# Optimization experiments

Measured on AMD Instinct MI355X. Metric: run time of the kernel, lower is better.

## Reference

```python
import jax, jax.numpy as jnp
import numpy as np

IMG = 128      # raster_settings.image_size
FOCAL = 1.5    # simple pinhole projection (camera transform)
EPS = 1e-8
B, V, F = 4, 600, 1000


def setup_inputs() -> dict:
    key = jax.random.key(0)
    k1, k2 = jax.random.split(key)
    u = jax.random.uniform(k1, (B, V, 3), dtype=jnp.float32)
    xy = u[..., :2] * 2.0 - 1.0          # x,y in [-1, 1]
    z = u[..., 2:3] * 2.0 + 1.0          # z in [1, 3] (in front of camera)
    verts = jnp.concatenate([xy, z], axis=-1)   # [B, V, 3] world coords
    faces = jax.random.randint(k2, (F, 3), 0, V)  # [F, 3] vertex indices
    return {"verts": verts, "faces": faces}


def _pix_grid(H, W):
    # PyTorch3D NDC convention: +X left, +Y up; pixel centers at (2i+1)/S - 1 flipped.
    xs = 1.0 - (2.0 * jnp.arange(W, dtype=jnp.float32) + 1.0) / W
    ys = 1.0 - (2.0 * jnp.arange(H, dtype=jnp.float32) + 1.0) / H
    px = jnp.broadcast_to(xs[None, :], (H, W)).reshape(-1)  # [P]
    py = jnp.broadcast_to(ys[:, None], (H, W)).reshape(-1)  # [P]
    return px, py


def _edge(ax, ay, bx, by, px, py):
    # signed (twice-)area of triangle (a, b, p)
    return (bx - ax) * (py - ay) - (by - ay) * (px - ax)


def _seg_dist2(px, py, ax, ay, bx, by):
    # squared distance from point p to segment (a, b); all args broadcastable
    ex, ey = bx - ax, by - ay
    dx, dy = px - ax, py - ay
    ee = jnp.maximum(ex * ex + ey * ey, EPS)
    t = jnp.clip((dx * ex + dy * ey) / ee, 0.0, 1.0)
    rx = dx - t * ex
    ry = dy - t * ey
    return rx * rx + ry * ry


def _rasterize_one(v_ndc, faces, H, W):
    fv = v_ndc[faces]                       # [F, 3, 3] face vertices (ndc x, y, view z)
    v0, v1, v2 = fv[:, 0], fv[:, 1], fv[:, 2]
    px, py = _pix_grid(H, W)                # [P], P = H*W
    pxr, pyr = px[None, :], py[None, :]
    # signed face area [F]
    area = _edge(v0[:, 0], v0[:, 1], v1[:, 0], v1[:, 1], v2[:, 0], v2[:, 1])
    # edge functions at every pixel -> unnormalized barycentrics [F, P]
    w0 = _edge(v1[:, 0:1], v1[:, 1:2], v2[:, 0:1], v2[:, 1:2], pxr, pyr)
    w1 = _edge(v2[:, 0:1], v2[:, 1:2], v0[:, 0:1], v0[:, 1:2], pxr, pyr)
    w2 = _edge(v0[:, 0:1], v0[:, 1:2], v1[:, 0:1], v1[:, 1:2], pxr, pyr)
    denom = jnp.where(jnp.abs(area) > EPS, area, EPS)[:, None]
    s0, s1, s2 = w0 / denom, w1 / denom, w2 / denom
    zpix = s0 * v0[:, 2:3] + s1 * v1[:, 2:3] + s2 * v2[:, 2:3]  # [F, P]
    inside = (s0 >= 0) & (s1 >= 0) & (s2 >= 0) \
             & (jnp.abs(area)[:, None] > EPS) & (zpix > 0)
    zcand = jnp.where(inside, zpix, jnp.inf)
    idx = jnp.argmin(zcand, axis=0)                       # [P] winning face per pixel
    gather = lambda a: jnp.take_along_axis(a, idx[None, :], axis=0)[0]
    zmin = gather(zcand)
    hit = jnp.isfinite(zmin)
    b0, b1, b2 = gather(s0), gather(s1), gather(s2)       # winner barycentrics [P]
    # signed squared point-triangle distance at the winning face (negative inside)
    fw = fv[idx]                                          # [P, 3, 3]
    a, b, c = fw[:, 0], fw[:, 1], fw[:, 2]
    d2 = jnp.minimum(
        jnp.minimum(_seg_dist2(px, py, a[:, 0], a[:, 1], b[:, 0], b[:, 1]),
                    _seg_dist2(px, py, b[:, 0], b[:, 1], c[:, 0], c[:, 1])),
        _seg_dist2(px, py, c[:, 0], c[:, 1], a[:, 0], a[:, 1]))
    pix_to_face = jnp.where(hit, idx, -1).reshape(H, W)
    zbuf = jnp.where(hit, zmin, -1.0).reshape(H, W)
    bary = jnp.where(hit[:, None], jnp.stack([b0, b1, b2], -1), -1.0).reshape(H, W, 3)
    dists = jnp.where(hit, -d2, -1.0).reshape(H, W)
    return pix_to_face, zbuf, bary, dists


def reference(verts, faces):
    # camera transform: identity world-to-view, perspective projection, keep view z
    x = FOCAL * verts[..., 0] / verts[..., 2]
    y = FOCAL * verts[..., 1] / verts[..., 2]
    v_ndc = jnp.stack([x, y, verts[..., 2]], axis=-1)     # [B, V, 3]
    rast = lambda v: _rasterize_one(v, faces, IMG, IMG)
    pix_to_face, zbuf, bary, dists = jax.vmap(rast)(v_ndc)
    return pix_to_face, zbuf, bary, dists
```

## Files before the change

### kernel.cpp

```cpp
#include <hip/hip_runtime.h>
#include <math.h>

namespace {

constexpr int IMG  = 128;
constexpr int NPIX = IMG * IMG;
constexpr int B    = 4;
constexpr int V    = 600;
constexpr int F    = 1000;
constexpr int FP   = 1024;
constexpr float FOCALF = 1.5f;
constexpr float EPSF   = 1e-8f;
constexpr float EW   = 1e-4f;
constexpr float EBIN = 2e-4f;
constexpr float DENSAFE = 1e-3f;

__device__ inline float seg_dist2(float px, float py, float ax, float ay,
                                  float bx, float by) {
#pragma clang fp contract(off)
    float ex = bx - ax, ey = by - ay;
    float dx = px - ax, dy = py - ay;
    float ee = fmaxf(ex * ex + ey * ey, EPSF);
    float t  = (dx * ex + dy * ey) / ee;
    t = fminf(fmaxf(t, 0.0f), 1.0f);
    float rx = dx - t * ex;
    float ry = dy - t * ey;
    return rx * rx + ry * ry;
}

__global__ __launch_bounds__(256) void setup_clear(const float* __restrict__ verts,
                                                   const int* __restrict__ faces,
                                                   float* __restrict__ fdata,
                                                   unsigned long long* __restrict__ zbest) {
#pragma clang fp contract(off)
    int t = blockIdx.x * 256 + threadIdx.x;
    zbest[t] = ~0ULL;
    if (t >= B * FP) return;
    const int b = t >> 10, fp = t & (FP - 1);
    float* o = fdata + (size_t)t * 28;
    bool dead = (fp >= F);
    float e0x=0,e0y=0,bx=0,by=0,e1x=0,e1y=0,cx=0,cy=0,e2x=0,e2y=0,ax=0,ay=0;
    float den=0, z0=0, z1=0, z2=0;
    if (!dead) {
        int i0 = faces[fp * 3 + 0], i1 = faces[fp * 3 + 1], i2 = faces[fp * 3 + 2];
        const float* vb = verts + (size_t)b * V * 3;
        float x0 = vb[i0 * 3], y0 = vb[i0 * 3 + 1]; z0 = vb[i0 * 3 + 2];
        float x1 = vb[i1 * 3], y1 = vb[i1 * 3 + 1]; z1 = vb[i1 * 3 + 2];
        float x2 = vb[i2 * 3], y2 = vb[i2 * 3 + 1]; z2 = vb[i2 * 3 + 2];
        ax = (FOCALF * x0) / z0; ay = (FOCALF * y0) / z0;
        bx = (FOCALF * x1) / z1; by = (FOCALF * y1) / z1;
        cx = (FOCALF * x2) / z2; cy = (FOCALF * y2) / z2;
        e0x = cx - bx; e0y = cy - by;
        e1x = ax - cx; e1y = ay - cy;
        e2x = bx - ax; e2y = by - ay;
        den = e2x * (cy - ay) - e2y * (cx - ax);
        if (!(fabsf(den) > EPSF)) { den = 0.0f; dead = true; }
    }
    if (dead) {
        o[0] = 0.0f; o[1] = 0.0f; o[2] = -1e30f; o[3] = 0.0f;
        #pragma unroll
        for (int k = 4; k < 28; ++k) o[k] = 0.0f;
        return;
    }
    float a0 = -e0y, b0 = e0x, c0 = e0y * bx - e0x * by;
    float a1 = -e1y, b1 = e1x, c1 = e1y * cx - e1x * cy;
    float a2 = -e2y, b2 = e2x, c2 = e2y * ax - e2x * ay;
    const float s  = den > 0.0f ? 1.0f : -1.0f;
    const float rd = __builtin_amdgcn_rcpf(den);
    const float azr = z0 * rd, bzr = z1 * rd, czr = z2 * rd;
    const float Zx = a0 * azr + a1 * bzr + a2 * czr;
    const float Zy = b0 * azr + b1 * bzr + b2 * czr;
    const float Zc = c0 * azr + c1 * bzr + c2 * czr;
    const float S = (fabsf(a0) + fabsf(b0) + fabsf(c0)) * fabsf(azr)
                  + (fabsf(a1) + fabsf(b1) + fabsf(c1)) * fabsf(bzr)
                  + (fabsf(a2) + fabsf(b2) + fabsf(c2)) * fabsf(czr);
    const float eps = (fabsf(den) < DENSAFE) ? INFINITY : (1e-4f + 2e-6f * S);
    o[0]  = s * a0; o[1]  = s * b0; o[2]  = s * c0; o[3]  = s * den;
    o[4]  = s * a1; o[5]  = s * b1; o[6]  = s * c1; o[7]  = eps;
    o[8]  = Zx;     o[9]  = Zy;     o[10] = Zc;     o[11] = 0.0f;
    o[12] = e0x;    o[13] = e0y;    o[14] = bx;     o[15] = by;
    o[16] = e1x;    o[17] = e1y;    o[18] = cx;     o[19] = cy;
    o[20] = e2x;    o[21] = e2y;    o[22] = ax;     o[23] = ay;
    o[24] = den;    o[25] = z0;     o[26] = z1;     o[27] = z2;
}

__global__ __launch_bounds__(512, 8) void rast(const float* __restrict__ fdata,
                                               unsigned long long* __restrict__ zbest) {
#pragma clang fp contract(off)
    __shared__ float4 sface[64 * 7];
    __shared__ unsigned int lticket;
    const int tid  = threadIdx.x;
    const int lane = tid & 63;
    const int bk   = blockIdx.x;
    const int ch   = bk & 15;
    const int b    = (bk >> 4) & 3;
    const int slice = bk >> 6;
    if (tid == 0) lticket = 0u;

    const int f0 = ch * 64;
    const float4* gflat = (const float4*)(fdata + (size_t)(b * FP + f0) * 28);
    if (tid < 448) ((float4*)sface)[tid] = gflat[tid];

    const float4* fd4 = (const float4*)(fdata + (size_t)(b * FP + f0 + lane) * 28);
    const float4 m0 = fd4[0], m1 = fd4[1];
    const float a2s = -(m0.x + m1.x);
    const float b2s = -(m0.y + m1.y);
    const float c2s = m0.w - m0.z - m1.z;
    const bool c0x = m0.x >= 0.0f, c0y = m0.y >= 0.0f;
    const bool c1x = m1.x >= 0.0f, c1y = m1.y >= 0.0f;
    const bool c2x = a2s >= 0.0f, c2y = b2s >= 0.0f;
    __syncthreads();

    const int dpx = lane & 7, dpy = lane >> 3;

    for (;;) {
        unsigned int j = 0;
        if (lane == 0) j = atomicAdd(&lticket, 1u);
        j = (unsigned int)__shfl((int)j, 0);
        if (j >= 16u) break;
        const unsigned int jj = (j + (unsigned int)ch) & 15u;

        const int row = (slice >> 2) + 4 * (int)(jj >> 2);
        const int col = (slice & 3) + 4 * (int)(jj & 3);
        const int ix0 = col * 8, iy0 = row * 8;
        const int ix  = ix0 + dpx, iy = iy0 + dpy;
        const float px = 1.0f - (2.0f * (float)ix + 1.0f) / (float)IMG;
        const float py = 1.0f - (2.0f * (float)iy + 1.0f) / (float)IMG;
        const float pxmax = 1.0f - (2.0f * (float)ix0 + 1.0f) / (float)IMG;
        const float pxmin = 1.0f - (2.0f * (float)(ix0 + 7) + 1.0f) / (float)IMG;
        const float pymax = 1.0f - (2.0f * (float)iy0 + 1.0f) / (float)IMG;
        const float pymin = 1.0f - (2.0f * (float)(iy0 + 7) + 1.0f) / (float)IMG;

        const int gp = b * NPIX + iy * IMG + ix;
        const unsigned ztop = (unsigned)(zbest[gp] >> 32);
        float zbf = (ztop == 0xFFFFFFFFu) ? INFINITY : __uint_as_float(ztop);

        bool pass =
            (m0.x * (c0x ? pxmax : pxmin) + m0.y * (c0y ? pymax : pymin) + m0.z)
                >= -EBIN;
        pass &=
            (m1.x * (c1x ? pxmax : pxmin) + m1.y * (c1y ? pymax : pymin) + m1.z)
                >= -EBIN;
        pass &=
            (a2s * (c2x ? pxmax : pxmin) + b2s * (c2y ? pymax : pymin) + c2s)
                >= -EBIN;

        unsigned long long pmin = ~0ULL;
        unsigned long long mask = __ballot(pass);
        while (mask) {
            const int sl = __builtin_ctzll(mask);
            mask &= mask - 1;
            const float4 k0 = sface[sl * 7 + 0];
            const float4 k1 = sface[sl * 7 + 1];
            const float g0 = fmaf(k0.x, px, fmaf(k0.y, py, k0.z));
            const float g1 = fmaf(k1.x, px, fmaf(k1.y, py, k1.z));
            const float g2 = k0.w - g0 - g1;
            const bool maybe = (g0 >= -EW) & (g1 >= -EW) & (g2 >= -EW);
            if (!__any(maybe)) continue;
            const float4 kz = sface[sl * 7 + 2];
            const float zt = fmaf(kz.x, px, fmaf(kz.y, py, kz.z));
            const bool need = maybe & (zt < zbf + k1.w);
            if (__any(need)) {
                const float4 r0 = sface[sl * 7 + 3];
                const float4 r1 = sface[sl * 7 + 4];
                const float4 r2 = sface[sl * 7 + 5];
                const float4 r3 = sface[sl * 7 + 6];
                const float den = r3.x;
                float w0 = r0.x * (py - r0.w) - r0.y * (px - r0.z);
                float w1 = r1.x * (py - r1.w) - r1.y * (px - r1.z);
                float w2 = r2.x * (py - r2.w) - r2.y * (px - r2.z);
                const unsigned ds = __float_as_uint(den) >> 31;
                const bool in0 = (w0 == 0.0f) | ((__float_as_uint(w0) >> 31) == ds);
                const bool in1 = (w1 == 0.0f) | ((__float_as_uint(w1) >> 31) == ds);
                const bool in2 = (w2 == 0.0f) | ((__float_as_uint(w2) >> 31) == ds);
                if (in0 & in1 & in2) {
                    float s0 = w0 / den, s1 = w1 / den, s2 = w2 / den;
                    float z  = s0 * r3.y + s1 * r3.z + s2 * r3.w;
                    if (z > 0.0f) {
                        unsigned long long pk =
                            ((unsigned long long)__float_as_uint(z) << 32) |
                            (unsigned)(f0 + sl);
                        pmin = pmin < pk ? pmin : pk;
                        zbf  = fminf(zbf, z);
                    }
                }
            }
        }
        if (pmin != ~0ULL) atomicMin(&zbest[gp], pmin);
    }
}

__global__ __launch_bounds__(256) void pass2(const float* __restrict__ fdata,
                                             const unsigned long long* __restrict__ zbest,
                                             float* __restrict__ out) {
#pragma clang fp contract(off)
    const int gp = blockIdx.x * 256 + threadIdx.x;
    const int b  = gp >> 14;
    const int p  = gp & (NPIX - 1);
    const int ix = p & (IMG - 1), iy = p >> 7;

    unsigned long long packed = zbest[gp];
    float o_face = -1.0f, o_z = -1.0f, o_b0 = -1.0f, o_b1 = -1.0f,
          o_b2 = -1.0f, o_d = -1.0f;

    if (packed != ~0ULL) {
        const int   idx = (int)(unsigned)(packed & 0xffffffffu);
        const float z   = __uint_as_float((unsigned)(packed >> 32));
        const float px  = 1.0f - (2.0f * (float)ix + 1.0f) / (float)IMG;
        const float py  = 1.0f - (2.0f * (float)iy + 1.0f) / (float)IMG;

        const float4* fd4 = (const float4*)(fdata + (size_t)(b * FP + idx) * 28);
        float4 q0 = fd4[3], q1 = fd4[4], q2 = fd4[5], q3 = fd4[6];
        float den = q3.x;
        float w0 = q0.x * (py - q0.w) - q0.y * (px - q0.z);
        float w1 = q1.x * (py - q1.w) - q1.y * (px - q1.z);
        float w2 = q2.x * (py - q2.w) - q2.y * (px - q2.z);
        float s0 = w0 / den, s1 = w1 / den, s2 = w2 / den;

        float d2 = fminf(fminf(seg_dist2(px, py, q2.z, q2.w, q0.z, q0.w),
                               seg_dist2(px, py, q0.z, q0.w, q1.z, q1.w)),
                         seg_dist2(px, py, q1.z, q1.w, q2.z, q2.w));
        o_face = (float)idx; o_z = z;
        o_b0 = s0; o_b1 = s1; o_b2 = s2;
        o_d = -d2;
    }

    out[gp]            = o_face;
    out[B * NPIX + gp] = o_z;
    const int bary_base = 2 * B * NPIX;
    out[bary_base + gp * 3 + 0] = o_b0;
    out[bary_base + gp * 3 + 1] = o_b1;
    out[bary_base + gp * 3 + 2] = o_b2;
    out[5 * B * NPIX + gp] = o_d;
}

}

extern "C" void kernel_launch(void* const* d_in, const int* in_sizes, int n_in,
                              void* d_out, int out_size, void* d_ws, size_t ws_size,
                              hipStream_t stream) {
    const float* verts = (const float*)d_in[0];
    const int*   faces = (const int*)d_in[1];
    float* out = (float*)d_out;

    char* ws = (char*)d_ws;
    unsigned long long* zbest = (unsigned long long*)ws;
    float* fdata = (float*)(ws + (size_t)B * NPIX * 8);

    setup_clear<<<B * NPIX / 256, 256, 0, stream>>>(verts, faces, fdata, zbest);
    rast<<<1024, 512, 0, stream>>>(fdata, zbest);
    pass2<<<B * NPIX / 256, 256, 0, stream>>>(fdata, zbest, out);
}
```

Before: 31.42 us.

## Fuse face setup into raster blocks, process two pixel rows per lane, recompute faces in pass2

Removes the separate setup kernel. Each raster block now projects its own 128 faces into shared memory, and zbest is cleared with hipMemsetAsync. Each lane covers two pixels (8x16 tiles), so the face records read from shared memory are reused across both pixels. Blocks drop to 256 threads with 128 faces per chunk. pass2 re-projects the winning face from verts and faces instead of reading a precomputed record, which adds redundant projection work per block and per pixel.

```diff
diff --git a/kernel.cpp b/kernel.cpp
--- a/kernel.cpp
+++ b/kernel.cpp
@@ -8,12 +8,38 @@
 constexpr int B    = 4;
 constexpr int V    = 600;
 constexpr int F    = 1000;
-constexpr int FP   = 1024;
 constexpr float FOCALF = 1.5f;
 constexpr float EPSF   = 1e-8f;
 constexpr float EW   = 1e-4f;
 constexpr float EBIN = 2e-4f;
 constexpr float DENSAFE = 1e-3f;
+
+struct FaceRec {
+    float e0x, e0y, bx, by;
+    float e1x, e1y, cx, cy;
+    float e2x, e2y, ax, ay;
+    float den, z0, z1, z2;
+};
+
+__device__ inline FaceRec project_face(const float* __restrict__ vb,
+                                       const int* __restrict__ faces, int f) {
+#pragma clang fp contract(off)
+    FaceRec r;
+    int i0 = faces[f * 3 + 0], i1 = faces[f * 3 + 1], i2 = faces[f * 3 + 2];
+    float x0 = vb[i0 * 3], y0 = vb[i0 * 3 + 1]; r.z0 = vb[i0 * 3 + 2];
+    float x1 = vb[i1 * 3], y1 = vb[i1 * 3 + 1]; r.z1 = vb[i1 * 3 + 2];
+    float x2 = vb[i2 * 3], y2 = vb[i2 * 3 + 1]; r.z2 = vb[i2 * 3 + 2];
+    r.ax = (FOCALF * x0) / r.z0; r.ay = (FOCALF * y0) / r.z0;
+    r.bx = (FOCALF * x1) / r.z1; r.by = (FOCALF * y1) / r.z1;
+    r.cx = (FOCALF * x2) / r.z2; r.cy = (FOCALF * y2) / r.z2;
+    r.e0x = r.cx - r.bx; r.e0y = r.cy - r.by;
+    r.e1x = r.ax - r.cx; r.e1y = r.ay - r.cy;
+    r.e2x = r.bx - r.ax; r.e2y = r.by - r.ay;
+    float den = r.e2x * (r.cy - r.ay) - r.e2y * (r.cx - r.ax);
+    if (!(fabsf(den) > EPSF)) den = 0.0f;
+    r.den = den;
+    return r;
+}
 
 __device__ inline float seg_dist2(float px, float py, float ax, float ay,
                                   float bx, float by) {
@@ -28,169 +54,194 @@
     return rx * rx + ry * ry;
 }
 
-__global__ __launch_bounds__(256) void setup_clear(const float* __restrict__ verts,
-                                                   const int* __restrict__ faces,
-                                                   float* __restrict__ fdata,
-                                                   unsigned long long* __restrict__ zbest) {
-#pragma clang fp contract(off)
-    int t = blockIdx.x * 256 + threadIdx.x;
-    zbest[t] = ~0ULL;
-    if (t >= B * FP) return;
-    const int b = t >> 10, fp = t & (FP - 1);
-    float* o = fdata + (size_t)t * 28;
-    bool dead = (fp >= F);
-    float e0x=0,e0y=0,bx=0,by=0,e1x=0,e1y=0,cx=0,cy=0,e2x=0,e2y=0,ax=0,ay=0;
-    float den=0, z0=0, z1=0, z2=0;
-    if (!dead) {
-        int i0 = faces[fp * 3 + 0], i1 = faces[fp * 3 + 1], i2 = faces[fp * 3 + 2];
-        const float* vb = verts + (size_t)b * V * 3;
-        float x0 = vb[i0 * 3], y0 = vb[i0 * 3 + 1]; z0 = vb[i0 * 3 + 2];
-        float x1 = vb[i1 * 3], y1 = vb[i1 * 3 + 1]; z1 = vb[i1 * 3 + 2];
-        float x2 = vb[i2 * 3], y2 = vb[i2 * 3 + 1]; z2 = vb[i2 * 3 + 2];
-        ax = (FOCALF * x0) / z0; ay = (FOCALF * y0) / z0;
-        bx = (FOCALF * x1) / z1; by = (FOCALF * y1) / z1;
-        cx = (FOCALF * x2) / z2; cy = (FOCALF * y2) / z2;
-        e0x = cx - bx; e0y = cy - by;
-        e1x = ax - cx; e1y = ay - cy;
-        e2x = bx - ax; e2y = by - ay;
-        den = e2x * (cy - ay) - e2y * (cx - ax);
-        if (!(fabsf(den) > EPSF)) { den = 0.0f; dead = true; }
-    }
-    if (dead) {
-        o[0] = 0.0f; o[1] = 0.0f; o[2] = -1e30f; o[3] = 0.0f;
-        #pragma unroll
-        for (int k = 4; k < 28; ++k) o[k] = 0.0f;
-        return;
-    }
-    float a0 = -e0y, b0 = e0x, c0 = e0y * bx - e0x * by;
-    float a1 = -e1y, b1 = e1x, c1 = e1y * cx - e1x * cy;
-    float a2 = -e2y, b2 = e2x, c2 = e2y * ax - e2x * ay;
-    const float s  = den > 0.0f ? 1.0f : -1.0f;
-    const float rd = __builtin_amdgcn_rcpf(den);
-    const float azr = z0 * rd, bzr = z1 * rd, czr = z2 * rd;
-    const float Zx = a0 * azr + a1 * bzr + a2 * czr;
-    const float Zy = b0 * azr + b1 * bzr + b2 * czr;
-    const float Zc = c0 * azr + c1 * bzr + c2 * czr;
-    const float S = (fabsf(a0) + fabsf(b0) + fabsf(c0)) * fabsf(azr)
-                  + (fabsf(a1) + fabsf(b1) + fabsf(c1)) * fabsf(bzr)
-                  + (fabsf(a2) + fabsf(b2) + fabsf(c2)) * fabsf(czr);
-    const float eps = (fabsf(den) < DENSAFE) ? INFINITY : (1e-4f + 2e-6f * S);
-    o[0]  = s * a0; o[1]  = s * b0; o[2]  = s * c0; o[3]  = s * den;
-    o[4]  = s * a1; o[5]  = s * b1; o[6]  = s * c1; o[7]  = eps;
-    o[8]  = Zx;     o[9]  = Zy;     o[10] = Zc;     o[11] = 0.0f;
-    o[12] = e0x;    o[13] = e0y;    o[14] = bx;     o[15] = by;
-    o[16] = e1x;    o[17] = e1y;    o[18] = cx;     o[19] = cy;
-    o[20] = e2x;    o[21] = e2y;    o[22] = ax;     o[23] = ay;
-    o[24] = den;    o[25] = z0;     o[26] = z1;     o[27] = z2;
-}
-
-__global__ __launch_bounds__(512, 8) void rast(const float* __restrict__ fdata,
+__global__ __launch_bounds__(256, 8) void rast(const float* __restrict__ verts,
+                                               const int* __restrict__ faces,
                                                unsigned long long* __restrict__ zbest) {
 #pragma clang fp contract(off)
-    __shared__ float4 sface[64 * 7];
+    __shared__ float4 sface[128 * 7];
     __shared__ unsigned int lticket;
     const int tid  = threadIdx.x;
     const int lane = tid & 63;
     const int bk   = blockIdx.x;
-    const int ch   = bk & 15;
-    const int b    = (bk >> 4) & 3;
-    const int slice = bk >> 6;
+    const int b     = bk & 3;
+    const int chgrp = (bk >> 2) & 7;
+    const int tg    = bk >> 5;
     if (tid == 0) lticket = 0u;
 
-    const int f0 = ch * 64;
-    const float4* gflat = (const float4*)(fdata + (size_t)(b * FP + f0) * 28);
-    if (tid < 448) ((float4*)sface)[tid] = gflat[tid];
-
-    const float4* fd4 = (const float4*)(fdata + (size_t)(b * FP + f0 + lane) * 28);
-    const float4 m0 = fd4[0], m1 = fd4[1];
-    const float a2s = -(m0.x + m1.x);
-    const float b2s = -(m0.y + m1.y);
-    const float c2s = m0.w - m0.z - m1.z;
-    const bool c0x = m0.x >= 0.0f, c0y = m0.y >= 0.0f;
-    const bool c1x = m1.x >= 0.0f, c1y = m1.y >= 0.0f;
-    const bool c2x = a2s >= 0.0f, c2y = b2s >= 0.0f;
+    if (tid < 128) {
+        const int fid = chgrp * 128 + tid;
+        float4 o0, o1, o2, o3, o4, o5, o6;
+        bool dead = (fid >= F);
+        FaceRec r = {};
+        if (!dead) {
+            r = project_face(verts + (size_t)b * V * 3, faces, fid);
+            dead = (r.den == 0.0f);
+        }
+        if (dead) {
+            o0 = make_float4(0.0f, 0.0f, -1e30f, 0.0f);
+            o1 = make_float4(0.0f, 0.0f, -1e30f, 0.0f);
+            o2 = make_float4(0.0f, 0.0f, 0.0f, 0.0f);
+            o3 = o4 = o5 = o6 = make_float4(0.0f, 0.0f, 0.0f, 0.0f);
+        } else {
+            float a0 = -r.e0y, b0 = r.e0x, c0 = r.e0y * r.bx - r.e0x * r.by;
+            float a1 = -r.e1y, b1 = r.e1x, c1 = r.e1y * r.cx - r.e1x * r.cy;
+            float a2 = -r.e2y, b2 = r.e2x, c2 = r.e2y * r.ax - r.e2x * r.ay;
+            const float s  = r.den > 0.0f ? 1.0f : -1.0f;
+            const float rd = __builtin_amdgcn_rcpf(r.den);
+            const float azr = r.z0 * rd, bzr = r.z1 * rd, czr = r.z2 * rd;
+            const float Zx = a0 * azr + a1 * bzr + a2 * czr;
+            const float Zy = b0 * azr + b1 * bzr + b2 * czr;
+            const float Zc = c0 * azr + c1 * bzr + c2 * czr;
+            const float S = (fabsf(a0) + fabsf(b0) + fabsf(c0)) * fabsf(azr)
+                          + (fabsf(a1) + fabsf(b1) + fabsf(c1)) * fabsf(bzr)
+                          + (fabsf(a2) + fabsf(b2) + fabsf(c2)) * fabsf(czr);
+            const float eps = (fabsf(r.den) < DENSAFE) ? INFINITY
+                                                       : (1e-4f + 2e-6f * S);
+            o0 = make_float4(s * a0, s * b0, s * c0, s * r.den);
+            o1 = make_float4(s * a1, s * b1, s * c1, eps);
+            o2 = make_float4(Zx, Zy, Zc, 0.0f);
+            o3 = make_float4(r.e0x, r.e0y, r.bx, r.by);
+            o4 = make_float4(r.e1x, r.e1y, r.cx, r.cy);
+            o5 = make_float4(r.e2x, r.e2y, r.ax, r.ay);
+            o6 = make_float4(r.den, r.z0, r.z1, r.z2);
+        }
+        float4* o = &sface[tid * 7];
+        o[0] = o0; o[1] = o1; o[2] = o2; o[3] = o3; o[4] = o4; o[5] = o5; o[6] = o6;
+    }
     __syncthreads();
 
+    float4 mm0[2], mm1[2];
+    mm0[0] = sface[lane * 7 + 0];        mm1[0] = sface[lane * 7 + 1];
+    mm0[1] = sface[(64 + lane) * 7 + 0]; mm1[1] = sface[(64 + lane) * 7 + 1];
+
+    const int r0g = tg >> 2, c0g = tg & 3;
     const int dpx = lane & 7, dpy = lane >> 3;
 
     for (;;) {
         unsigned int j = 0;
         if (lane == 0) j = atomicAdd(&lticket, 1u);
         j = (unsigned int)__shfl((int)j, 0);
-        if (j >= 16u) break;
-        const unsigned int jj = (j + (unsigned int)ch) & 15u;
-
-        const int row = (slice >> 2) + 4 * (int)(jj >> 2);
-        const int col = (slice & 3) + 4 * (int)(jj & 3);
-        const int ix0 = col * 8, iy0 = row * 8;
-        const int ix  = ix0 + dpx, iy = iy0 + dpy;
-        const float px = 1.0f - (2.0f * (float)ix + 1.0f) / (float)IMG;
-        const float py = 1.0f - (2.0f * (float)iy + 1.0f) / (float)IMG;
+        if (j >= 8u) break;
+        const unsigned int jj = (j + (unsigned int)chgrp) & 7u;
+
+        const int row = r0g + 4 * (int)(jj >> 2);
+        const int col = c0g + 4 * (int)(jj & 3);
+        const int ix0 = col * 8, iy0 = row * 16;
+        const int ix  = ix0 + dpx;
+        const int iyA = iy0 + dpy, iyB = iyA + 8;
+        const float px  = 1.0f - (2.0f * (float)ix  + 1.0f) / (float)IMG;
+        const float pyA = 1.0f - (2.0f * (float)iyA + 1.0f) / (float)IMG;
+        const float pyB = 1.0f - (2.0f * (float)iyB + 1.0f) / (float)IMG;
         const float pxmax = 1.0f - (2.0f * (float)ix0 + 1.0f) / (float)IMG;
         const float pxmin = 1.0f - (2.0f * (float)(ix0 + 7) + 1.0f) / (float)IMG;
         const float pymax = 1.0f - (2.0f * (float)iy0 + 1.0f) / (float)IMG;
-        const float pymin = 1.0f - (2.0f * (float)(iy0 + 7) + 1.0f) / (float)IMG;
-
-        const int gp = b * NPIX + iy * IMG + ix;
-        const unsigned ztop = (unsigned)(zbest[gp] >> 32);
-        float zbf = (ztop == 0xFFFFFFFFu) ? INFINITY : __uint_as_float(ztop);
-
-        bool pass =
-            (m0.x * (c0x ? pxmax : pxmin) + m0.y * (c0y ? pymax : pymin) + m0.z)
-                >= -EBIN;
-        pass &=
-            (m1.x * (c1x ? pxmax : pxmin) + m1.y * (c1y ? pymax : pymin) + m1.z)
-                >= -EBIN;
-        pass &=
-            (a2s * (c2x ? pxmax : pxmin) + b2s * (c2y ? pymax : pymin) + c2s)
-                >= -EBIN;
-
-        unsigned long long pmin = ~0ULL;
-        unsigned long long mask = __ballot(pass);
-        while (mask) {
-            const int sl = __builtin_ctzll(mask);
-            mask &= mask - 1;
-            const float4 k0 = sface[sl * 7 + 0];
-            const float4 k1 = sface[sl * 7 + 1];
-            const float g0 = fmaf(k0.x, px, fmaf(k0.y, py, k0.z));
-            const float g1 = fmaf(k1.x, px, fmaf(k1.y, py, k1.z));
-            const float g2 = k0.w - g0 - g1;
-            const bool maybe = (g0 >= -EW) & (g1 >= -EW) & (g2 >= -EW);
-            if (!__any(maybe)) continue;
-            const float4 kz = sface[sl * 7 + 2];
-            const float zt = fmaf(kz.x, px, fmaf(kz.y, py, kz.z));
-            const bool need = maybe & (zt < zbf + k1.w);
-            if (__any(need)) {
-                const float4 r0 = sface[sl * 7 + 3];
-                const float4 r1 = sface[sl * 7 + 4];
-                const float4 r2 = sface[sl * 7 + 5];
-                const float4 r3 = sface[sl * 7 + 6];
-                const float den = r3.x;
-                float w0 = r0.x * (py - r0.w) - r0.y * (px - r0.z);
-                float w1 = r1.x * (py - r1.w) - r1.y * (px - r1.z);
-                float w2 = r2.x * (py - r2.w) - r2.y * (px - r2.z);
-                const unsigned ds = __float_as_uint(den) >> 31;
-                const bool in0 = (w0 == 0.0f) | ((__float_as_uint(w0) >> 31) == ds);
-                const bool in1 = (w1 == 0.0f) | ((__float_as_uint(w1) >> 31) == ds);
-                const bool in2 = (w2 == 0.0f) | ((__float_as_uint(w2) >> 31) == ds);
-                if (in0 & in1 & in2) {
-                    float s0 = w0 / den, s1 = w1 / den, s2 = w2 / den;
-                    float z  = s0 * r3.y + s1 * r3.z + s2 * r3.w;
-                    if (z > 0.0f) {
-                        unsigned long long pk =
-                            ((unsigned long long)__float_as_uint(z) << 32) |
-                            (unsigned)(f0 + sl);
-                        pmin = pmin < pk ? pmin : pk;
-                        zbf  = fminf(zbf, z);
+        const float pymin = 1.0f - (2.0f * (float)(iy0 + 15) + 1.0f) / (float)IMG;
+
+        const int gpA = b * NPIX + iyA * IMG + ix;
+        const int gpB = gpA + 8 * IMG;
+        const unsigned ztopA = (unsigned)(zbest[gpA] >> 32);
+        const unsigned ztopB = (unsigned)(zbest[gpB] >> 32);
+        float zA = (ztopA == 0xFFFFFFFFu) ? INFINITY : __uint_as_float(ztopA);
+        float zB = (ztopB == 0xFFFFFFFFu) ? INFINITY : __uint_as_float(ztopB);
+
+        unsigned long long pminA = ~0ULL, pminB = ~0ULL;
+
+        #pragma unroll
+        for (int k = 0; k < 2; ++k) {
+            const float4 m0 = mm0[k], m1 = mm1[k];
+            const float a2s = -(m0.x + m1.x);
+            const float b2s = -(m0.y + m1.y);
+            const float c2s = m0.w - m0.z - m1.z;
+            bool pass =
+                (m0.x * (m0.x >= 0.0f ? pxmax : pxmin)
+               + m0.y * (m0.y >= 0.0f ? pymax : pymin) + m0.z) >= -EBIN;
+            pass &=
+                (m1.x * (m1.x >= 0.0f ? pxmax : pxmin)
+               + m1.y * (m1.y >= 0.0f ? pymax : pymin) + m1.z) >= -EBIN;
+            pass &=
+                (a2s * (a2s >= 0.0f ? pxmax : pxmin)
+               + b2s * (b2s >= 0.0f ? pymax : pymin) + c2s) >= -EBIN;
+
+            unsigned long long mask = __ballot(pass);
+            const int base = k * 64;
+            while (mask) {
+                const int sl = __builtin_ctzll(mask);
+                mask &= mask - 1;
+                const float4 k0 = sface[(base + sl) * 7 + 0];
+                const float4 k1 = sface[(base + sl) * 7 + 1];
+                const float g0A = fmaf(k0.x, px, fmaf(k0.y, pyA, k0.z));
+                const float g1A = fmaf(k1.x, px, fmaf(k1.y, pyA, k1.z));
+                const float g2A = k0.w - g0A - g1A;
+                const float g0B = fmaf(k0.x, px, fmaf(k0.y, pyB, k0.z));
+                const float g1B = fmaf(k1.x, px, fmaf(k1.y, pyB, k1.z));
+                const float g2B = k0.w - g0B - g1B;
+                const bool mayA = (g0A >= -EW) & (g1A >= -EW) & (g2A >= -EW);
+                const bool mayB = (g0B >= -EW) & (g1B >= -EW) & (g2B >= -EW);
+                if (!__any(mayA | mayB)) continue;
+                const float4 kz = sface[(base + sl) * 7 + 2];
+                const float ztA = fmaf(kz.x, px, fmaf(kz.y, pyA, kz.z));
+                const float ztB = fmaf(kz.x, px, fmaf(kz.y, pyB, kz.z));
+                const bool needA = mayA & (ztA < zA + k1.w);
+                const bool needB = mayB & (ztB < zB + k1.w);
+                if (__any(needA)) {
+                    const float4 r0 = sface[(base + sl) * 7 + 3];
+                    const float4 r1 = sface[(base + sl) * 7 + 4];
+                    const float4 r2 = sface[(base + sl) * 7 + 5];
+                    const float4 r3 = sface[(base + sl) * 7 + 6];
+                    const float den = r3.x;
+                    float w0 = r0.x * (pyA - r0.w) - r0.y * (px - r0.z);
+                    float w1 = r1.x * (pyA - r1.w) - r1.y * (px - r1.z);
+                    float w2 = r2.x * (pyA - r2.w) - r2.y * (px - r2.z);
+                    const unsigned ds = __float_as_uint(den) >> 31;
+                    const bool in0 = (w0 == 0.0f) | ((__float_as_uint(w0) >> 31) == ds);
+                    const bool in1 = (w1 == 0.0f) | ((__float_as_uint(w1) >> 31) == ds);
+                    const bool in2 = (w2 == 0.0f) | ((__float_as_uint(w2) >> 31) == ds);
+                    if (in0 & in1 & in2) {
+                        float s0 = w0 / den, s1 = w1 / den, s2 = w2 / den;
+                        float z  = s0 * r3.y + s1 * r3.z + s2 * r3.w;
+                        if (z > 0.0f) {
+                            unsigned long long pk =
+                                ((unsigned long long)__float_as_uint(z) << 32) |
+                                (unsigned)(chgrp * 128 + base + sl);
+                            pminA = pminA < pk ? pminA : pk;
+                            zA = fminf(zA, z);
+                        }
+                    }
+                }
+                if (__any(needB)) {
+                    const float4 r0 = sface[(base + sl) * 7 + 3];
+                    const float4 r1 = sface[(base + sl) * 7 + 4];
+                    const float4 r2 = sface[(base + sl) * 7 + 5];
+                    const float4 r3 = sface[(base + sl) * 7 + 6];
+                    const float den = r3.x;
+                    float w0 = r0.x * (pyB - r0.w) - r0.y * (px - r0.z);
+                    float w1 = r1.x * (pyB - r1.w) - r1.y * (px - r1.z);
+                    float w2 = r2.x * (pyB - r2.w) - r2.y * (px - r2.z);
+                    const unsigned ds = __float_as_uint(den) >> 31;
+                    const bool in0 = (w0 == 0.0f) | ((__float_as_uint(w0) >> 31) == ds);
+                    const bool in1 = (w1 == 0.0f) | ((__float_as_uint(w1) >> 31) == ds);
+                    const bool in2 = (w2 == 0.0f) | ((__float_as_uint(w2) >> 31) == ds);
+                    if (in0 & in1 & in2) {
+                        float s0 = w0 / den, s1 = w1 / den, s2 = w2 / den;
+                        float z  = s0 * r3.y + s1 * r3.z + s2 * r3.w;
+                        if (z > 0.0f) {
+                            unsigned long long pk =
+                                ((unsigned long long)__float_as_uint(z) << 32) |
+                                (unsigned)(chgrp * 128 + base + sl);
+                            pminB = pminB < pk ? pminB : pk;
+                            zB = fminf(zB, z);
+                        }
                     }
                 }
             }
         }
-        if (pmin != ~0ULL) atomicMin(&zbest[gp], pmin);
+        if (pminA != ~0ULL) atomicMin(&zbest[gpA], pminA);
+        if (pminB != ~0ULL) atomicMin(&zbest[gpB], pminB);
     }
 }
 
-__global__ __launch_bounds__(256) void pass2(const float* __restrict__ fdata,
+__global__ __launch_bounds__(256) void pass2(const float* __restrict__ verts,
+                                             const int* __restrict__ faces,
                                              const unsigned long long* __restrict__ zbest,
                                              float* __restrict__ out) {
 #pragma clang fp contract(off)
@@ -209,17 +260,15 @@
         const float px  = 1.0f - (2.0f * (float)ix + 1.0f) / (float)IMG;
         const float py  = 1.0f - (2.0f * (float)iy + 1.0f) / (float)IMG;
 
-        const float4* fd4 = (const float4*)(fdata + (size_t)(b * FP + idx) * 28);
-        float4 q0 = fd4[3], q1 = fd4[4], q2 = fd4[5], q3 = fd4[6];
-        float den = q3.x;
-        float w0 = q0.x * (py - q0.w) - q0.y * (px - q0.z);
-        float w1 = q1.x * (py - q1.w) - q1.y * (px - q1.z);
-        float w2 = q2.x * (py - q2.w) - q2.y * (px - q2.z);
-        float s0 = w0 / den, s1 = w1 / den, s2 = w2 / den;
-
-        float d2 = fminf(fminf(seg_dist2(px, py, q2.z, q2.w, q0.z, q0.w),
-                               seg_dist2(px, py, q0.z, q0.w, q1.z, q1.w)),
-                         seg_dist2(px, py, q1.z, q1.w, q2.z, q2.w));
+        FaceRec r = project_face(verts + (size_t)b * V * 3, faces, idx);
+        float w0 = r.e0x * (py - r.by) - r.e0y * (px - r.bx);
+        float w1 = r.e1x * (py - r.cy) - r.e1y * (px - r.cx);
+        float w2 = r.e2x * (py - r.ay) - r.e2y * (px - r.ax);
+        float s0 = w0 / r.den, s1 = w1 / r.den, s2 = w2 / r.den;
+
+        float d2 = fminf(fminf(seg_dist2(px, py, r.ax, r.ay, r.bx, r.by),
+                               seg_dist2(px, py, r.bx, r.by, r.cx, r.cy)),
+                         seg_dist2(px, py, r.cx, r.cy, r.ax, r.ay));
         o_face = (float)idx; o_z = z;
         o_b0 = s0; o_b1 = s1; o_b2 = s2;
         o_d = -d2;
@@ -243,11 +292,9 @@
     const int*   faces = (const int*)d_in[1];
     float* out = (float*)d_out;
 
-    char* ws = (char*)d_ws;
-    unsigned long long* zbest = (unsigned long long*)ws;
-    float* fdata = (float*)(ws + (size_t)B * NPIX * 8);
-
-    setup_clear<<<B * NPIX / 256, 256, 0, stream>>>(verts, faces, fdata, zbest);
-    rast<<<1024, 512, 0, stream>>>(fdata, zbest);
-    pass2<<<B * NPIX / 256, 256, 0, stream>>>(fdata, zbest, out);
-}
+    unsigned long long* zbest = (unsigned long long*)d_ws;
+
+    hipMemsetAsync(zbest, 0xFF, (size_t)B * NPIX * 8, stream);
+    rast<<<512, 256, 0, stream>>>(verts, faces, zbest);
+    pass2<<<B * NPIX / 256, 256, 0, stream>>>(verts, faces, zbest, out);
+}
```

Result: slower. 44.06 us (+40.2%).

## Assign each block one pixel tile, reduce depth in LDS, fuse resolve pass

Applied to the files above, without the earlier changes.

The rasterizer now gives each block one 8x8 pixel tile and lets its eight waves pull 64-face chunks from a block-local ticket. The per-pixel depth minimum is kept in shared memory, so the global zbest buffer, its clear and the separate resolve kernel all go away. The final barycentric and distance outputs are written from the same kernel, which saves a launch and global atomics. In exchange, only 64 threads of the block do the epilogue, the expensive face data is read from global memory rather than LDS, and the depth-based early rejection depends on shared-memory atomics from other waves.

```diff
diff --git a/kernel.cpp b/kernel.cpp
--- a/kernel.cpp
+++ b/kernel.cpp
@@ -28,18 +28,17 @@
     return rx * rx + ry * ry;
 }
 
-__global__ __launch_bounds__(256) void setup_clear(const float* __restrict__ verts,
-                                                   const int* __restrict__ faces,
-                                                   float* __restrict__ fdata,
-                                                   unsigned long long* __restrict__ zbest) {
+__global__ __launch_bounds__(256) void setup(const float* __restrict__ verts,
+                                             const int* __restrict__ faces,
+                                             float* __restrict__ fdata) {
 #pragma clang fp contract(off)
     int t = blockIdx.x * 256 + threadIdx.x;
-    zbest[t] = ~0ULL;
     if (t >= B * FP) return;
     const int b = t >> 10, fp = t & (FP - 1);
     float* o = fdata + (size_t)t * 28;
     bool dead = (fp >= F);
-    float e0x=0,e0y=0,bx=0,by=0,e1x=0,e1y=0,cx=0,cy=0,e2x=0,e2y=0,ax=0,ay=0;
+    float ax=0,ay=0,bx=0,by=0,cx=0,cy=0;
+    float e0x=0,e0y=0,e1x=0,e1y=0,e2x=0,e2y=0;
     float den=0, z0=0, z1=0, z2=0;
     if (!dead) {
         int i0 = faces[fp * 3 + 0], i1 = faces[fp * 3 + 1], i2 = faces[fp * 3 + 2];
@@ -58,8 +57,9 @@
     }
     if (dead) {
         o[0] = 0.0f; o[1] = 0.0f; o[2] = -1e30f; o[3] = 0.0f;
+        o[4] = 0.0f; o[5] = 0.0f; o[6] = -1e30f; o[7] = 0.0f;
         #pragma unroll
-        for (int k = 4; k < 28; ++k) o[k] = 0.0f;
+        for (int k = 8; k < 28; ++k) o[k] = 0.0f;
         return;
     }
     float a0 = -e0y, b0 = e0x, c0 = e0y * bx - e0x * by;
@@ -85,86 +85,80 @@
 }
 
 __global__ __launch_bounds__(512, 8) void rast(const float* __restrict__ fdata,
-                                               unsigned long long* __restrict__ zbest) {
+                                               float* __restrict__ out) {
 #pragma clang fp contract(off)
-    __shared__ float4 sface[64 * 7];
+    __shared__ float4 scheap[8][64][3];
+    __shared__ unsigned long long tilebest[64];
     __shared__ unsigned int lticket;
     const int tid  = threadIdx.x;
     const int lane = tid & 63;
+    const int w    = tid >> 6;
     const int bk   = blockIdx.x;
-    const int ch   = bk & 15;
-    const int b    = (bk >> 4) & 3;
-    const int slice = bk >> 6;
+    const int b    = bk >> 8;
+    const int t    = bk & 255;
+    const int ix0  = (t & 15) * 8, iy0 = (t >> 4) * 8;
+    if (tid < 64) tilebest[tid] = ~0ULL;
     if (tid == 0) lticket = 0u;
-
-    const int f0 = ch * 64;
-    const float4* gflat = (const float4*)(fdata + (size_t)(b * FP + f0) * 28);
-    if (tid < 448) ((float4*)sface)[tid] = gflat[tid];
-
-    const float4* fd4 = (const float4*)(fdata + (size_t)(b * FP + f0 + lane) * 28);
-    const float4 m0 = fd4[0], m1 = fd4[1];
-    const float a2s = -(m0.x + m1.x);
-    const float b2s = -(m0.y + m1.y);
-    const float c2s = m0.w - m0.z - m1.z;
-    const bool c0x = m0.x >= 0.0f, c0y = m0.y >= 0.0f;
-    const bool c1x = m1.x >= 0.0f, c1y = m1.y >= 0.0f;
-    const bool c2x = a2s >= 0.0f, c2y = b2s >= 0.0f;
     __syncthreads();
 
     const int dpx = lane & 7, dpy = lane >> 3;
+    const int ix = ix0 + dpx, iy = iy0 + dpy;
+    const float px = 1.0f - (2.0f * (float)ix + 1.0f) / (float)IMG;
+    const float py = 1.0f - (2.0f * (float)iy + 1.0f) / (float)IMG;
+    const float pxmax = 1.0f - (2.0f * (float)ix0 + 1.0f) / (float)IMG;
+    const float pxmin = 1.0f - (2.0f * (float)(ix0 + 7) + 1.0f) / (float)IMG;
+    const float pymax = 1.0f - (2.0f * (float)iy0 + 1.0f) / (float)IMG;
+    const float pymin = 1.0f - (2.0f * (float)(iy0 + 7) + 1.0f) / (float)IMG;
+
+    const volatile unsigned* tb_hi = (const volatile unsigned*)tilebest;
 
     for (;;) {
-        unsigned int j = 0;
-        if (lane == 0) j = atomicAdd(&lticket, 1u);
-        j = (unsigned int)__shfl((int)j, 0);
-        if (j >= 16u) break;
-        const unsigned int jj = (j + (unsigned int)ch) & 15u;
-
-        const int row = (slice >> 2) + 4 * (int)(jj >> 2);
-        const int col = (slice & 3) + 4 * (int)(jj & 3);
-        const int ix0 = col * 8, iy0 = row * 8;
-        const int ix  = ix0 + dpx, iy = iy0 + dpy;
-        const float px = 1.0f - (2.0f * (float)ix + 1.0f) / (float)IMG;
-        const float py = 1.0f - (2.0f * (float)iy + 1.0f) / (float)IMG;
-        const float pxmax = 1.0f - (2.0f * (float)ix0 + 1.0f) / (float)IMG;
-        const float pxmin = 1.0f - (2.0f * (float)(ix0 + 7) + 1.0f) / (float)IMG;
-        const float pymax = 1.0f - (2.0f * (float)iy0 + 1.0f) / (float)IMG;
-        const float pymin = 1.0f - (2.0f * (float)(iy0 + 7) + 1.0f) / (float)IMG;
-
-        const int gp = b * NPIX + iy * IMG + ix;
-        const unsigned ztop = (unsigned)(zbest[gp] >> 32);
-        float zbf = (ztop == 0xFFFFFFFFu) ? INFINITY : __uint_as_float(ztop);
-
+        unsigned int c = 0;
+        if (lane == 0) c = atomicAdd(&lticket, 1u);
+        c = (unsigned int)__shfl((int)c, 0);
+        if (c >= 16u) break;
+        const int fbase = (int)c * 64;
+
+        const float4* fp4 =
+            (const float4*)(fdata + (size_t)(b * FP + fbase + lane) * 28);
+        const float4 m0 = fp4[0], m1 = fp4[1], m2 = fp4[2];
+        scheap[w][lane][0] = m0;
+        scheap[w][lane][1] = m1;
+        scheap[w][lane][2] = m2;
+
+        const float a2s = -(m0.x + m1.x);
+        const float b2s = -(m0.y + m1.y);
+        const float c2s = m0.w - m0.z - m1.z;
         bool pass =
-            (m0.x * (c0x ? pxmax : pxmin) + m0.y * (c0y ? pymax : pymin) + m0.z)
-                >= -EBIN;
+            (m0.x * (m0.x >= 0.0f ? pxmax : pxmin)
+           + m0.y * (m0.y >= 0.0f ? pymax : pymin) + m0.z) >= -EBIN;
         pass &=
-            (m1.x * (c1x ? pxmax : pxmin) + m1.y * (c1y ? pymax : pymin) + m1.z)
-                >= -EBIN;
+            (m1.x * (m1.x >= 0.0f ? pxmax : pxmin)
+           + m1.y * (m1.y >= 0.0f ? pymax : pymin) + m1.z) >= -EBIN;
         pass &=
-            (a2s * (c2x ? pxmax : pxmin) + b2s * (c2y ? pymax : pymin) + c2s)
-                >= -EBIN;
-
-        unsigned long long pmin = ~0ULL;
+            (a2s * (a2s >= 0.0f ? pxmax : pxmin)
+           + b2s * (b2s >= 0.0f ? pymax : pymin) + c2s) >= -EBIN;
+
         unsigned long long mask = __ballot(pass);
         while (mask) {
             const int sl = __builtin_ctzll(mask);
             mask &= mask - 1;
-            const float4 k0 = sface[sl * 7 + 0];
-            const float4 k1 = sface[sl * 7 + 1];
+            const float4 k0 = scheap[w][sl][0];
+            const float4 k1 = scheap[w][sl][1];
             const float g0 = fmaf(k0.x, px, fmaf(k0.y, py, k0.z));
             const float g1 = fmaf(k1.x, px, fmaf(k1.y, py, k1.z));
             const float g2 = k0.w - g0 - g1;
             const bool maybe = (g0 >= -EW) & (g1 >= -EW) & (g2 >= -EW);
             if (!__any(maybe)) continue;
-            const float4 kz = sface[sl * 7 + 2];
+            const float4 kz = scheap[w][sl][2];
             const float zt = fmaf(kz.x, px, fmaf(kz.y, py, kz.z));
+            const unsigned u = tb_hi[lane * 2 + 1];
+            const float zbf = (u == 0xFFFFFFFFu) ? INFINITY : __uint_as_float(u);
             const bool need = maybe & (zt < zbf + k1.w);
             if (__any(need)) {
-                const float4 r0 = sface[sl * 7 + 3];
-                const float4 r1 = sface[sl * 7 + 4];
-                const float4 r2 = sface[sl * 7 + 5];
-                const float4 r3 = sface[sl * 7 + 6];
+                const float4* fe =
+                    (const float4*)(fdata + (size_t)(b * FP + fbase + sl) * 28);
+                const float4 r0 = fe[3], r1 = fe[4], r2 = fe[5], r3 = fe[6];
                 const float den = r3.x;
                 float w0 = r0.x * (py - r0.w) - r0.y * (px - r0.z);
                 float w1 = r1.x * (py - r1.w) - r1.y * (px - r1.z);
@@ -179,59 +173,49 @@
                     if (z > 0.0f) {
                         unsigned long long pk =
                             ((unsigned long long)__float_as_uint(z) << 32) |
-                            (unsigned)(f0 + sl);
-                        pmin = pmin < pk ? pmin : pk;
-                        zbf  = fminf(zbf, z);
+                            (unsigned)(fbase + sl);
+                        atomicMin(&tilebest[lane], pk);
                     }
                 }
             }
         }
-        if (pmin != ~0ULL) atomicMin(&zbest[gp], pmin);
-    }
-}
-
-__global__ __launch_bounds__(256) void pass2(const float* __restrict__ fdata,
-                                             const unsigned long long* __restrict__ zbest,
-                                             float* __restrict__ out) {
-#pragma clang fp contract(off)
-    const int gp = blockIdx.x * 256 + threadIdx.x;
-    const int b  = gp >> 14;
-    const int p  = gp & (NPIX - 1);
-    const int ix = p & (IMG - 1), iy = p >> 7;
-
-    unsigned long long packed = zbest[gp];
-    float o_face = -1.0f, o_z = -1.0f, o_b0 = -1.0f, o_b1 = -1.0f,
-          o_b2 = -1.0f, o_d = -1.0f;
-
-    if (packed != ~0ULL) {
-        const int   idx = (int)(unsigned)(packed & 0xffffffffu);
-        const float z   = __uint_as_float((unsigned)(packed >> 32));
-        const float px  = 1.0f - (2.0f * (float)ix + 1.0f) / (float)IMG;
-        const float py  = 1.0f - (2.0f * (float)iy + 1.0f) / (float)IMG;
-
-        const float4* fd4 = (const float4*)(fdata + (size_t)(b * FP + idx) * 28);
-        float4 q0 = fd4[3], q1 = fd4[4], q2 = fd4[5], q3 = fd4[6];
-        float den = q3.x;
-        float w0 = q0.x * (py - q0.w) - q0.y * (px - q0.z);
-        float w1 = q1.x * (py - q1.w) - q1.y * (px - q1.z);
-        float w2 = q2.x * (py - q2.w) - q2.y * (px - q2.z);
-        float s0 = w0 / den, s1 = w1 / den, s2 = w2 / den;
-
-        float d2 = fminf(fminf(seg_dist2(px, py, q2.z, q2.w, q0.z, q0.w),
-                               seg_dist2(px, py, q0.z, q0.w, q1.z, q1.w)),
-                         seg_dist2(px, py, q1.z, q1.w, q2.z, q2.w));
-        o_face = (float)idx; o_z = z;
-        o_b0 = s0; o_b1 = s1; o_b2 = s2;
-        o_d = -d2;
-    }
-
-    out[gp]            = o_face;
-    out[B * NPIX + gp] = o_z;
-    const int bary_base = 2 * B * NPIX;
-    out[bary_base + gp * 3 + 0] = o_b0;
-    out[bary_base + gp * 3 + 1] = o_b1;
-    out[bary_base + gp * 3 + 2] = o_b2;
-    out[5 * B * NPIX + gp] = o_d;
+    }
+    __syncthreads();
+
+    if (tid < 64) {
+        const int eix = ix0 + (tid & 7), eiy = iy0 + (tid >> 3);
+        const int gp  = b * NPIX + eiy * IMG + eix;
+        const unsigned long long packed = tilebest[tid];
+        float o_face = -1.0f, o_z = -1.0f, o_b0 = -1.0f, o_b1 = -1.0f,
+              o_b2 = -1.0f, o_d = -1.0f;
+        if (packed != ~0ULL) {
+            const int   idx = (int)(unsigned)(packed & 0xffffffffu);
+            const float z   = __uint_as_float((unsigned)(packed >> 32));
+            const float epx = 1.0f - (2.0f * (float)eix + 1.0f) / (float)IMG;
+            const float epy = 1.0f - (2.0f * (float)eiy + 1.0f) / (float)IMG;
+            const float4* fe =
+                (const float4*)(fdata + (size_t)(b * FP + idx) * 28);
+            const float4 q0 = fe[3], q1 = fe[4], q2 = fe[5], q3 = fe[6];
+            float den = q3.x;
+            float w0 = q0.x * (epy - q0.w) - q0.y * (epx - q0.z);
+            float w1 = q1.x * (epy - q1.w) - q1.y * (epx - q1.z);
+            float w2 = q2.x * (epy - q2.w) - q2.y * (epx - q2.z);
+            float s0 = w0 / den, s1 = w1 / den, s2 = w2 / den;
+            float d2 = fminf(fminf(seg_dist2(epx, epy, q2.z, q2.w, q0.z, q0.w),
+                                   seg_dist2(epx, epy, q0.z, q0.w, q1.z, q1.w)),
+                             seg_dist2(epx, epy, q1.z, q1.w, q2.z, q2.w));
+            o_face = (float)idx; o_z = z;
+            o_b0 = s0; o_b1 = s1; o_b2 = s2;
+            o_d = -d2;
+        }
+        out[gp]            = o_face;
+        out[B * NPIX + gp] = o_z;
+        const int bary_base = 2 * B * NPIX;
+        out[bary_base + gp * 3 + 0] = o_b0;
+        out[bary_base + gp * 3 + 1] = o_b1;
+        out[bary_base + gp * 3 + 2] = o_b2;
+        out[5 * B * NPIX + gp] = o_d;
+    }
 }
 
 }
@@ -243,11 +227,8 @@
     const int*   faces = (const int*)d_in[1];
     float* out = (float*)d_out;
 
-    char* ws = (char*)d_ws;
-    unsigned long long* zbest = (unsigned long long*)ws;
-    float* fdata = (float*)(ws + (size_t)B * NPIX * 8);
-
-    setup_clear<<<B * NPIX / 256, 256, 0, stream>>>(verts, faces, fdata, zbest);
-    rast<<<1024, 512, 0, stream>>>(fdata, zbest);
-    pass2<<<B * NPIX / 256, 256, 0, stream>>>(fdata, zbest, out);
-}
+    float* fdata = (float*)d_ws;
+
+    setup<<<B * FP / 256, 256, 0, stream>>>(verts, faces, fdata);
+    rast<<<1024, 512, 0, stream>>>(fdata, out);
+}
```

Result: slower. 36.91 us (+17.5%).
